# Optimization experiments

Measured on AMD Instinct MI355X. Metric: run time of the kernel, lower is better.

The kernel has to match this reference:

```python
import jax, jax.numpy as jnp
import numpy as np

B, S, D_IN, D_OUT = 8, 2048, 512, 512


def setup_inputs() -> dict:
    key = jax.random.key(0)
    ks = jax.random.split(key, 6)
    return {
        "inputs_for_keys": jax.random.normal(ks[0], (B, S, D_IN), dtype=jnp.float32),
        "inputs_for_values": jax.random.normal(ks[1], (B, S, D_IN), dtype=jnp.float32),
        "inputs_for_queries": jax.random.normal(ks[2], (B, S, D_IN), dtype=jnp.float32),
        "Wq": jax.random.normal(ks[3], (D_IN, D_OUT), dtype=jnp.float32) * 0.05,
        "Wk": jax.random.normal(ks[4], (D_IN, D_OUT), dtype=jnp.float32) * 0.05,
        "Wv": jax.random.normal(ks[5], (D_IN, D_OUT), dtype=jnp.float32) * 0.05,
    }


def reference(inputs_for_keys, inputs_for_values, inputs_for_queries, Wq, Wk, Wv):
    # Projections: [B,S,D_in] @ [D_in,D_out] -> [B,S,D_out]
    Q = inputs_for_queries @ Wq
    K = inputs_for_keys @ Wk
    V = inputs_for_values @ Wv
    d_k = K.shape[-1]
    scale = 1.0 / jnp.sqrt(jnp.float32(d_k))
    # Scores: [B,Sq,Sk]
    scores = jnp.einsum("bqd,bkd->bqk", Q, K) * scale
    # Causal mask: original adds -inf for key positions j > query i (use_mask=True)
    q_idx = jnp.arange(Q.shape[1])[:, None]
    k_idx = jnp.arange(K.shape[1])[None, :]
    scores = jnp.where(k_idx > q_idx, jnp.float32(-jnp.inf), scores)
    attn = jax.nn.softmax(scores, axis=-1)
    return jnp.einsum("bqk,bkd->bqd", attn, V)
```

## Files before the change

### kernel.cpp

```cpp
#include <hip/hip_runtime.h>
#include <hip/hip_bf16.h>

typedef __bf16 bf16;
typedef __bf16 bf16x4 __attribute__((ext_vector_type(4)));
typedef __bf16 bf16x8 __attribute__((ext_vector_type(8)));
typedef float f32x4 __attribute__((ext_vector_type(4)));
typedef float f32x16 __attribute__((ext_vector_type(16)));

#define NB 8
#define NS 2048
#define ND 512

static __device__ __forceinline__ f32x4 mfma16(bf16x8 a, bf16x8 b, f32x4 c) {
  return __builtin_amdgcn_mfma_f32_16x16x32_bf16(a, b, c, 0, 0, 0);
}
static __device__ __forceinline__ f32x16 mfma32(bf16x8 a, bf16x8 b, f32x16 c) {
  return __builtin_amdgcn_mfma_f32_32x32x16_bf16(a, b, c, 0, 0, 0);
}
static __device__ __forceinline__ void async16(const bf16* g, bf16* l) {
  __builtin_amdgcn_global_load_lds((const __attribute__((address_space(1))) void*)g,
                                   (__attribute__((address_space(3))) void*)l, 16, 0, 0);
}

#define WAVE_VM0() asm volatile("s_waitcnt vmcnt(0)" ::: "memory")
#define BLK_BAR() do { asm volatile("s_waitcnt lgkmcnt(0)" ::: "memory"); \
  __builtin_amdgcn_s_barrier(); __builtin_amdgcn_sched_barrier(0); } while (0)

__global__ void wconv_kernel(const float* __restrict__ Wq,
                             const float* __restrict__ Wk,
                             const float* __restrict__ Wv,
                             bf16* __restrict__ Wt) {
  __shared__ float buf[64][65];
  const int z = blockIdx.z;
  const float* W = (z == 0) ? Wq : (z == 1) ? Wk : Wv;
  const float scale = (z == 0) ? 0.063763537f : 1.0f;
  const int k0 = blockIdx.x * 64, n0 = blockIdx.y * 64;
  const int t = threadIdx.x;
#pragma unroll
  for (int i = 0; i < 16; ++i) {
    int idx = i * 256 + t;
    int kk = idx >> 6, nn = idx & 63;
    buf[kk][nn] = W[(size_t)(k0 + kk) * 512 + n0 + nn];
  }
  __syncthreads();
#pragma unroll
  for (int i = 0; i < 16; ++i) {
    int idx = i * 256 + t;
    int nn = idx >> 6, kk = idx & 63;
    Wt[(size_t)z * 262144 + (size_t)(n0 + nn) * 512 + k0 + (kk ^ ((nn & 7) << 3))] =
        (bf16)(buf[kk][nn] * scale);
  }
}

__launch_bounds__(256)
__global__ void proj_kernel(const float* __restrict__ Xq,
                            const float* __restrict__ Xk,
                            const float* __restrict__ Xv,
                            const bf16* __restrict__ Wt,
                            bf16* __restrict__ Cq,
                            bf16* __restrict__ Ck,
                            bf16* __restrict__ Cv) {
  __shared__ bf16 As[2][128][72];
  __shared__ bf16 WsL[2][8192];
  const int z = blockIdx.z;
  const float* A = (z == 0) ? Xq : (z == 1) ? Xk : Xv;
  const bf16* Wz = Wt + (size_t)z * 262144;
  bf16* C = (z == 0) ? Cq : (z == 1) ? Ck : Cv;

  const int t = threadIdx.x;
  const int lane = t & 63;
  const int w = t >> 6;
  const int wr = w >> 1, wc = w & 1;
  const int bxr = blockIdx.x;
  const int mt = (bxr & 7) * 16 + (bxr >> 3);
  const int bm = mt * 128;
  const int bn = blockIdx.y * 128;
  const int r0 = t >> 4, seg = t & 15;

  f32x4 acc[4][4] = {};
  float4 ar[8];

  auto loadA = [&](int kc) {
#pragma unroll
    for (int p = 0; p < 8; ++p)
      ar[p] = *(const float4*)(A + (size_t)(bm + p * 16 + r0) * 512 + kc * 64 + seg * 4);
  };
  auto writeA = [&](int bufi) {
#pragma unroll
    for (int p = 0; p < 8; ++p) {
      bf16x4 o = {(bf16)ar[p].x, (bf16)ar[p].y, (bf16)ar[p].z, (bf16)ar[p].w};
      *(bf16x4*)&As[bufi][p * 16 + r0][seg * 4] = o;
    }
  };
  auto issueW = [&](int kc, int bufi) {
    const int n = t >> 3, sg8 = t & 7;
#pragma unroll
    for (int i = 0; i < 4; ++i)
      async16(Wz + (size_t)(bn + i * 32 + n) * 512 + kc * 64 + sg8 * 8,
              &WsL[bufi][(i * 32 + n) * 64 + sg8 * 8]);
  };

  loadA(0);
  WAVE_VM0();
  writeA(0);
  issueW(0, 0);
  loadA(1);
  asm volatile("s_waitcnt vmcnt(8) lgkmcnt(0)" ::: "memory");
  __builtin_amdgcn_s_barrier();
  __builtin_amdgcn_sched_barrier(0);

#pragma unroll
  for (int kc = 0; kc < 8; ++kc) {
    const int c = kc & 1;
    if (kc < 7) issueW(kc + 1, c ^ 1);
    const int arow = lane & 15, kq = (lane >> 4) * 8;
#pragma unroll
    for (int kk = 0; kk < 2; ++kk) {
      bf16x8 af[4], bfr[4];
#pragma unroll
      for (int mi = 0; mi < 4; ++mi)
        af[mi] = *(const bf16x8*)&As[c][wr * 64 + mi * 16 + arow][kk * 32 + kq];
#pragma unroll
      for (int ni = 0; ni < 4; ++ni) {
        int n = wc * 64 + ni * 16 + arow;
        bfr[ni] = *(const bf16x8*)&WsL[c][n * 64 + ((kk * 32 + kq) ^ ((n & 7) << 3))];
      }
#pragma unroll
      for (int mi = 0; mi < 4; ++mi)
#pragma unroll
        for (int ni = 0; ni < 4; ++ni)
          acc[mi][ni] = mfma16(af[mi], bfr[ni], acc[mi][ni]);
    }
    if (kc < 7) {
      asm volatile("s_waitcnt vmcnt(4)" ::: "memory");
      writeA(c ^ 1);
      if (kc < 6) {
        loadA(kc + 2);
        asm volatile("s_waitcnt vmcnt(8) lgkmcnt(0)" ::: "memory");
      } else {
        asm volatile("s_waitcnt vmcnt(0) lgkmcnt(0)" ::: "memory");
      }
      __builtin_amdgcn_s_barrier();
      __builtin_amdgcn_sched_barrier(0);
    }
  }

  const int row0 = (lane >> 4) * 4, col = lane & 15;
#pragma unroll
  for (int mi = 0; mi < 4; ++mi)
#pragma unroll
    for (int ni = 0; ni < 4; ++ni) {
      int cg = bn + wc * 64 + ni * 16 + col;
#pragma unroll
      for (int j = 0; j < 4; ++j) {
        int rg = bm + wr * 64 + mi * 16 + row0 + j;
        bf16 o = (bf16)acc[mi][ni][j];
        if (z == 0) {
          C[(size_t)rg * ND + cg] = o;
        } else if (z == 1) {
          C[(size_t)rg * ND + (cg ^ ((rg & 7) << 3))] = o;
        } else {
          int bb = rg >> 11, s = rg & 2047;
          int ss = (s & ~63) | ((s & 63) ^ ((cg & 7) << 3));
          C[(size_t)bb * (ND * NS) + (size_t)cg * NS + ss] = o;
        }
      }
    }
}

__launch_bounds__(512, 2)
__global__ void attn_kernel(const bf16* __restrict__ Qg,
                            const bf16* __restrict__ Kg,
                            const bf16* __restrict__ Vtg,
                            bf16* __restrict__ Pn,
                            float* __restrict__ Mp,
                            float* __restrict__ Lp) {
  __shared__ bf16 Ks[64][512];
  __shared__ bf16 Vts[512][64];
  __shared__ bf16 Sx[64][68];
  __shared__ bf16 Ps[2][64][76];
  __shared__ float r_lds[2][64];
  __shared__ float l_lds[64];

  const int t = threadIdx.x;
  const int lane = t & 63;
  const int w = t >> 6;
  const int l31 = lane & 31, lhi = lane >> 5;
  const int wq = w & 3;
  const bool isQK = w < 4;
  const int qh = wq & 1, skh = wq >> 1;
  const int dofs = wq * 128;

  const int id = blockIdx.x;
  const int b = id & 7;
  const int qt = 31 - ((id >> 3) & 31);
  const int h = id >> 8;
  const int q0 = qt * 64;
  const int nt = qt + 1, mid = (nt + 1) >> 1;
  const int t_begin = h ? mid : 0;
  const int t_end = h ? nt : mid;
  const int NT = t_end - t_begin;
  const int pidx = (h * 8 + b) * 32 + qt;

  const bf16* Qb = Qg + (size_t)b * NS * ND;
  const bf16* Kb = Kg + (size_t)b * NS * ND;
  const bf16* Vb = Vtg + (size_t)b * ND * NS;

  if (isQK) {
    const int ql = qh * 32 + l31;
    const int qg = q0 + ql;
    bf16x8 qf[16];
    float m_run = -1e30f, l_run = 0.0f;
    if (NT > 0) {
      const bf16* qrow = Qb + (size_t)qg * ND + skh * 256 + lhi * 8;
#pragma unroll
      for (int kc = 0; kc < 16; ++kc) qf[kc] = *(const bf16x8*)(qrow + kc * 16);
#pragma unroll
      for (int i = 0; i < 16; ++i)
        async16(Kb + (size_t)(t_begin * 64 + wq * 16 + i) * ND + lane * 8,
                &Ks[wq * 16 + i][0]);
    }
    for (int s = 0; s <= NT; ++s) {
      const int it = t_begin + s;
      f32x16 s0 = {}, s1 = {};
      if (s < NT) WAVE_VM0();
      BLK_BAR();
      if (s < NT) {
        __builtin_amdgcn_s_setprio(1);
#pragma unroll
        for (int kc = 0; kc < 16; ++kc) {
          const int colk = (skh * 256 + kc * 16 + lhi * 8) ^ ((l31 & 7) << 3);
          bf16x8 kf0 = *(const bf16x8*)&Ks[l31][colk];
          bf16x8 kf1 = *(const bf16x8*)&Ks[32 + l31][colk];
          s0 = mfma32(kf0, qf[kc], s0);
          s1 = mfma32(kf1, qf[kc], s1);
        }
        __builtin_amdgcn_s_setprio(0);
        if (skh) {
#pragma unroll
          for (int jg = 0; jg < 4; ++jg) {
            bf16x4 a = {(bf16)s0[jg * 4 + 0], (bf16)s0[jg * 4 + 1],
                        (bf16)s0[jg * 4 + 2], (bf16)s0[jg * 4 + 3]};
            bf16x4 c = {(bf16)s1[jg * 4 + 0], (bf16)s1[jg * 4 + 1],
                        (bf16)s1[jg * 4 + 2], (bf16)s1[jg * 4 + 3]};
            *(bf16x4*)&Sx[ql][jg * 8 + 4 * lhi] = a;
            *(bf16x4*)&Sx[ql][32 + jg * 8 + 4 * lhi] = c;
          }
        }
      }
      BLK_BAR();
      if (s < NT) {
        if (it + 1 < t_end) {
#pragma unroll
          for (int i = 0; i < 16; ++i)
            async16(Kb + (size_t)((it + 1) * 64 + wq * 16 + i) * ND + lane * 8,
                    &Ks[wq * 16 + i][0]);
        }
        if (!skh) {
          float v[32];
#pragma unroll
          for (int jg = 0; jg < 4; ++jg) {
            bf16x4 a = *(const bf16x4*)&Sx[ql][jg * 8 + 4 * lhi];
            bf16x4 c = *(const bf16x4*)&Sx[ql][32 + jg * 8 + 4 * lhi];
#pragma unroll
            for (int e = 0; e < 4; ++e) {
              v[jg * 4 + e] = s0[jg * 4 + e] + (float)a[e];
              v[16 + jg * 4 + e] = s1[jg * 4 + e] + (float)c[e];
            }
          }
          if (it == qt) {
            const int k0 = it * 64;
#pragma unroll
            for (int j = 0; j < 16; ++j) {
              int kv = k0 + (j & 3) + 8 * (j >> 2) + 4 * lhi;
              if (kv > qg) v[j] = -1e30f;
              if (kv + 32 > qg) v[16 + j] = -1e30f;
            }
          }
          float mx = v[0];
#pragma unroll
          for (int j = 1; j < 32; ++j) mx = fmaxf(mx, v[j]);
          mx = fmaxf(mx, __shfl_xor(mx, 32));
          float mn = fmaxf(m_run, mx);
          float rr = exp2f(m_run - mn);
          float sum = 0.0f;
#pragma unroll
          for (int j = 0; j < 32; ++j) { v[j] = exp2f(v[j] - mn); sum += v[j]; }
          sum += __shfl_xor(sum, 32);
          m_run = mn;
          l_run = l_run * rr + sum;
          if (lhi == 0) r_lds[it & 1][ql] = rr;
#pragma unroll
          for (int jg = 0; jg < 4; ++jg) {
            bf16x4 a = {(bf16)v[jg * 4 + 0], (bf16)v[jg * 4 + 1],
                        (bf16)v[jg * 4 + 2], (bf16)v[jg * 4 + 3]};
            bf16x4 c = {(bf16)v[16 + jg * 4 + 0], (bf16)v[16 + jg * 4 + 1],
                        (bf16)v[16 + jg * 4 + 2], (bf16)v[16 + jg * 4 + 3]};
            *(bf16x4*)&Ps[it & 1][ql][jg * 8 + 4 * lhi] = a;
            *(bf16x4*)&Ps[it & 1][ql][32 + jg * 8 + 4 * lhi] = c;
          }
        }
      }
    }
    if (!skh && lhi == 0) {
      Mp[pidx * 64 + ql] = m_run;
      Lp[pidx * 64 + ql] = l_run;
      l_lds[ql] = l_run;
    }
    BLK_BAR();
  } else {
    f32x16 acc[2][4] = {};
    if (NT > 0) {
#pragma unroll
      for (int i = 0; i < 16; ++i) {
        int d = dofs + i * 8 + (lane >> 3);
        async16(Vb + (size_t)d * NS + t_begin * 64 + (lane & 7) * 8,
                &Vts[dofs + i * 8][0]);
      }
    }
    for (int s = 0; s <= NT; ++s) {
      const int it = t_begin + s;
      if (s >= 1) WAVE_VM0();
      BLK_BAR();
      bf16x8 paf[2][4];
      if (s >= 1) {
        const int bb = (it - 1) & 1;
#pragma unroll
        for (int qb = 0; qb < 2; ++qb)
#pragma unroll
          for (int j = 0; j < 16; ++j) {
            float rr = r_lds[bb][qb * 32 + (j & 3) + 8 * (j >> 2) + 4 * lhi];
#pragma unroll
            for (int dt = 0; dt < 4; ++dt) acc[qb][dt][j] *= rr;
          }
#pragma unroll
        for (int qb = 0; qb < 2; ++qb)
#pragma unroll
          for (int kc = 0; kc < 4; ++kc)
            paf[qb][kc] = *(const bf16x8*)&Ps[bb][qb * 32 + l31][kc * 16 + lhi * 8];
        __builtin_amdgcn_s_setprio(1);
#pragma unroll
        for (int dt = 0; dt < 2; ++dt) {
          const int d = dofs + dt * 32 + l31;
          const int swzv = (d & 7) << 3;
#pragma unroll
          for (int kc = 0; kc < 4; ++kc) {
            bf16x8 vf = *(const bf16x8*)&Vts[d][(kc * 16 + lhi * 8) ^ swzv];
            acc[0][dt] = mfma32(paf[0][kc], vf, acc[0][dt]);
            acc[1][dt] = mfma32(paf[1][kc], vf, acc[1][dt]);
          }
        }
        __builtin_amdgcn_s_setprio(0);
      }
      BLK_BAR();
      if (s >= 1) {
        __builtin_amdgcn_s_setprio(1);
#pragma unroll
        for (int dt = 2; dt < 4; ++dt) {
          const int d = dofs + dt * 32 + l31;
          const int swzv = (d & 7) << 3;
#pragma unroll
          for (int kc = 0; kc < 4; ++kc) {
            bf16x8 vf = *(const bf16x8*)&Vts[d][(kc * 16 + lhi * 8) ^ swzv];
            acc[0][dt] = mfma32(paf[0][kc], vf, acc[0][dt]);
            acc[1][dt] = mfma32(paf[1][kc], vf, acc[1][dt]);
          }
        }
        __builtin_amdgcn_s_setprio(0);
        asm volatile("s_waitcnt lgkmcnt(0)" ::: "memory");
        if (it < t_end) {
#pragma unroll
          for (int i = 0; i < 16; ++i) {
            int d = dofs + i * 8 + (lane >> 3);
            async16(Vb + (size_t)d * NS + it * 64 + (lane & 7) * 8,
                    &Vts[dofs + i * 8][0]);
          }
        }
      }
    }
    BLK_BAR();
    bf16* Ob = Pn + (size_t)pidx * 64 * ND;
#pragma unroll
    for (int qb = 0; qb < 2; ++qb)
#pragma unroll
      for (int j = 0; j < 16; ++j) {
        const int row = qb * 32 + (j & 3) + 8 * (j >> 2) + 4 * lhi;
        float lv = l_lds[row];
        float linv = (lv > 0.0f) ? 1.0f / lv : 0.0f;
#pragma unroll
        for (int dt = 0; dt < 4; ++dt)
          Ob[(size_t)row * ND + dofs + dt * 32 + l31] = (bf16)(acc[qb][dt][j] * linv);
      }
  }
}

__global__ void combine_kernel(const bf16* __restrict__ Pn,
                               const float* __restrict__ Mp,
                               const float* __restrict__ Lp,
                               float* __restrict__ Out) {
  const int total = NB * NS * ND / 4;
  for (int v = blockIdx.x * 256 + threadIdx.x; v < total; v += gridDim.x * 256) {
    int e = v * 4;
    int d = e & 511;
    int s = (e >> 9) & 2047;
    int bb = e >> 20;
    int qt = s >> 6, r = s & 63;
    int p0 = (bb * 32 + qt) * 64 + r;
    int p1 = ((8 + bb) * 32 + qt) * 64 + r;
    float m0 = Mp[p0], l0 = Lp[p0], m1 = Mp[p1], l1 = Lp[p1];
    float M = fmaxf(m0, m1);
    float w0 = l0 * exp2f(m0 - M), w1 = l1 * exp2f(m1 - M);
    float inv = 1.0f / (w0 + w1);
    bf16x4 o0 = *(const bf16x4*)(Pn + (size_t)p0 * ND + d);
    bf16x4 o1 = *(const bf16x4*)(Pn + (size_t)p1 * ND + d);
    f32x4 o;
    o[0] = (w0 * (float)o0[0] + w1 * (float)o1[0]) * inv;
    o[1] = (w0 * (float)o0[1] + w1 * (float)o1[1]) * inv;
    o[2] = (w0 * (float)o0[2] + w1 * (float)o1[2]) * inv;
    o[3] = (w0 * (float)o0[3] + w1 * (float)o1[3]) * inv;
    __builtin_nontemporal_store(o, (f32x4*)(Out + e));
  }
}

extern "C" void kernel_launch(void* const* d_in, const int* in_sizes, int n_in,
                              void* d_out, int out_size, void* d_ws, size_t ws_size,
                              hipStream_t stream) {
  const float* Xk = (const float*)d_in[0];
  const float* Xv = (const float*)d_in[1];
  const float* Xq = (const float*)d_in[2];
  const float* Wq = (const float*)d_in[3];
  const float* Wk = (const float*)d_in[4];
  const float* Wv = (const float*)d_in[5];
  float* Out = (float*)d_out;

  char* ws = (char*)d_ws;
  bf16* Qb = (bf16*)(ws);
  bf16* Kb = (bf16*)(ws + (size_t)16 * 1024 * 1024);
  bf16* Vt = (bf16*)(ws + (size_t)32 * 1024 * 1024);
  bf16* Wt = (bf16*)(ws + (size_t)48 * 1024 * 1024);
  bf16* Pn = (bf16*)(ws + (size_t)50 * 1024 * 1024);
  float* Mp = (float*)(ws + (size_t)82 * 1024 * 1024);
  float* Lp = (float*)(ws + (size_t)82 * 1024 * 1024 + 131072);

  wconv_kernel<<<dim3(8, 8, 3), 256, 0, stream>>>(Wq, Wk, Wv, Wt);
  proj_kernel<<<dim3(128, 4, 3), 256, 0, stream>>>(Xq, Xk, Xv, Wt, Qb, Kb, Vt);
  attn_kernel<<<512, 512, 0, stream>>>(Qb, Kb, Vt, Pn, Mp, Lp);
  combine_kernel<<<2048, 256, 0, stream>>>(Pn, Mp, Lp, Out);
}
```

Before: 146.8 us.

## Split only long query tiles across blocks and repartition QK waves by key half

The work split now depends on tile length. Query tiles 0-15 run as a single block that writes fp32 output directly. Tiles 16-31 are split into two KV halves that still go through the combine kernel, so the grid drops to 384 blocks and combine only handles the upper half of the sequence. The QK waves now each compute a 32-key half over the full head dimension and exchange per-row max and sum through LDS. This removes the bf16 partial-score exchange and the serial softmax on half the waves. Each QK wave now keeps twice as many Q fragments in registers, and the launch bound drops to one block per SM, which may reduce occupancy.

```diff
diff --git a/kernel.cpp b/kernel.cpp
--- a/kernel.cpp
+++ b/kernel.cpp
@@ -168,17 +168,18 @@
     }
 }
 
-__launch_bounds__(512, 2)
+__launch_bounds__(512, 1)
 __global__ void attn_kernel(const bf16* __restrict__ Qg,
                             const bf16* __restrict__ Kg,
                             const bf16* __restrict__ Vtg,
+                            float* __restrict__ Out,
                             bf16* __restrict__ Pn,
                             float* __restrict__ Mp,
                             float* __restrict__ Lp) {
   __shared__ bf16 Ks[64][512];
   __shared__ bf16 Vts[512][64];
-  __shared__ bf16 Sx[64][68];
   __shared__ bf16 Ps[2][64][76];
+  __shared__ float2 Mx[2][64];
   __shared__ float r_lds[2][64];
   __shared__ float l_lds[64];
 
@@ -188,19 +189,24 @@
   const int l31 = lane & 31, lhi = lane >> 5;
   const int wq = w & 3;
   const bool isQK = w < 4;
-  const int qh = wq & 1, skh = wq >> 1;
+  const int qh = wq & 1, kvh = wq >> 1;
   const int dofs = wq * 128;
 
   const int id = blockIdx.x;
   const int b = id & 7;
-  const int qt = 31 - ((id >> 3) & 31);
-  const int h = id >> 8;
+  const int g = id >> 3;
+  const int j3 = g / 3, r3 = g - 3 * j3;
+  int qt, t_begin, t_end, mode;
+  if (r3 == 0) { qt = 15 - j3; t_begin = 0; t_end = qt + 1; mode = 0; }
+  else {
+    qt = 31 - j3;
+    int mid = (qt + 2) >> 1;
+    if (r3 == 1) { t_begin = 0; t_end = mid; mode = 1; }
+    else { t_begin = mid; t_end = qt + 1; mode = 2; }
+  }
   const int q0 = qt * 64;
-  const int nt = qt + 1, mid = (nt + 1) >> 1;
-  const int t_begin = h ? mid : 0;
-  const int t_end = h ? nt : mid;
   const int NT = t_end - t_begin;
-  const int pidx = (h * 8 + b) * 32 + qt;
+  const int pidx = ((mode == 2 ? 8 : 0) + b) * 32 + qt;
 
   const bf16* Qb = Qg + (size_t)b * NS * ND;
   const bf16* Kb = Kg + (size_t)b * NS * ND;
@@ -209,44 +215,49 @@
   if (isQK) {
     const int ql = qh * 32 + l31;
     const int qg = q0 + ql;
-    bf16x8 qf[16];
+    bf16x8 qf[32];
     float m_run = -1e30f, l_run = 0.0f;
-    if (NT > 0) {
-      const bf16* qrow = Qb + (size_t)qg * ND + skh * 256 + lhi * 8;
-#pragma unroll
-      for (int kc = 0; kc < 16; ++kc) qf[kc] = *(const bf16x8*)(qrow + kc * 16);
+    {
+      const bf16* qrow = Qb + (size_t)qg * ND + lhi * 8;
+#pragma unroll
+      for (int kc = 0; kc < 32; ++kc) qf[kc] = *(const bf16x8*)(qrow + kc * 16);
 #pragma unroll
       for (int i = 0; i < 16; ++i)
         async16(Kb + (size_t)(t_begin * 64 + wq * 16 + i) * ND + lane * 8,
                 &Ks[wq * 16 + i][0]);
     }
+    const int swz = (l31 & 7) << 3;
+    const int krow = kvh * 32 + l31;
     for (int s = 0; s <= NT; ++s) {
       const int it = t_begin + s;
-      f32x16 s0 = {}, s1 = {};
+      f32x16 sacc = {};
       if (s < NT) WAVE_VM0();
       BLK_BAR();
+      float m_loc = -1e30f, sum_loc = 0.0f, p[16];
       if (s < NT) {
         __builtin_amdgcn_s_setprio(1);
 #pragma unroll
-        for (int kc = 0; kc < 16; ++kc) {
-          const int colk = (skh * 256 + kc * 16 + lhi * 8) ^ ((l31 & 7) << 3);
-          bf16x8 kf0 = *(const bf16x8*)&Ks[l31][colk];
-          bf16x8 kf1 = *(const bf16x8*)&Ks[32 + l31][colk];
-          s0 = mfma32(kf0, qf[kc], s0);
-          s1 = mfma32(kf1, qf[kc], s1);
+        for (int kc = 0; kc < 32; ++kc) {
+          bf16x8 kf = *(const bf16x8*)&Ks[krow][(kc * 16 + lhi * 8) ^ swz];
+          sacc = mfma32(kf, qf[kc], sacc);
         }
         __builtin_amdgcn_s_setprio(0);
-        if (skh) {
-#pragma unroll
-          for (int jg = 0; jg < 4; ++jg) {
-            bf16x4 a = {(bf16)s0[jg * 4 + 0], (bf16)s0[jg * 4 + 1],
-                        (bf16)s0[jg * 4 + 2], (bf16)s0[jg * 4 + 3]};
-            bf16x4 c = {(bf16)s1[jg * 4 + 0], (bf16)s1[jg * 4 + 1],
-                        (bf16)s1[jg * 4 + 2], (bf16)s1[jg * 4 + 3]};
-            *(bf16x4*)&Sx[ql][jg * 8 + 4 * lhi] = a;
-            *(bf16x4*)&Sx[ql][32 + jg * 8 + 4 * lhi] = c;
-          }
-        }
+        float v[16];
+#pragma unroll
+        for (int j = 0; j < 16; ++j) v[j] = sacc[j];
+        if (it == qt && mode != 1) {
+          const int kvb = it * 64 + kvh * 32;
+#pragma unroll
+          for (int j = 0; j < 16; ++j)
+            if (kvb + (j & 3) + 8 * (j >> 2) + 4 * lhi > qg) v[j] = -1e30f;
+        }
+#pragma unroll
+        for (int j = 0; j < 16; ++j) m_loc = fmaxf(m_loc, v[j]);
+        m_loc = fmaxf(m_loc, __shfl_xor(m_loc, 32));
+#pragma unroll
+        for (int j = 0; j < 16; ++j) { p[j] = exp2f(v[j] - m_loc); sum_loc += p[j]; }
+        sum_loc += __shfl_xor(sum_loc, 32);
+        if (lhi == 0) Mx[kvh][ql] = {m_loc, sum_loc};
       }
       BLK_BAR();
       if (s < NT) {
@@ -256,61 +267,30 @@
             async16(Kb + (size_t)((it + 1) * 64 + wq * 16 + i) * ND + lane * 8,
                     &Ks[wq * 16 + i][0]);
         }
-        if (!skh) {
-          float v[32];
-#pragma unroll
-          for (int jg = 0; jg < 4; ++jg) {
-            bf16x4 a = *(const bf16x4*)&Sx[ql][jg * 8 + 4 * lhi];
-            bf16x4 c = *(const bf16x4*)&Sx[ql][32 + jg * 8 + 4 * lhi];
-#pragma unroll
-            for (int e = 0; e < 4; ++e) {
-              v[jg * 4 + e] = s0[jg * 4 + e] + (float)a[e];
-              v[16 + jg * 4 + e] = s1[jg * 4 + e] + (float)c[e];
-            }
-          }
-          if (it == qt) {
-            const int k0 = it * 64;
-#pragma unroll
-            for (int j = 0; j < 16; ++j) {
-              int kv = k0 + (j & 3) + 8 * (j >> 2) + 4 * lhi;
-              if (kv > qg) v[j] = -1e30f;
-              if (kv + 32 > qg) v[16 + j] = -1e30f;
-            }
-          }
-          float mx = v[0];
-#pragma unroll
-          for (int j = 1; j < 32; ++j) mx = fmaxf(mx, v[j]);
-          mx = fmaxf(mx, __shfl_xor(mx, 32));
-          float mn = fmaxf(m_run, mx);
-          float rr = exp2f(m_run - mn);
-          float sum = 0.0f;
-#pragma unroll
-          for (int j = 0; j < 32; ++j) { v[j] = exp2f(v[j] - mn); sum += v[j]; }
-          sum += __shfl_xor(sum, 32);
-          m_run = mn;
-          l_run = l_run * rr + sum;
-          if (lhi == 0) r_lds[it & 1][ql] = rr;
-#pragma unroll
-          for (int jg = 0; jg < 4; ++jg) {
-            bf16x4 a = {(bf16)v[jg * 4 + 0], (bf16)v[jg * 4 + 1],
-                        (bf16)v[jg * 4 + 2], (bf16)v[jg * 4 + 3]};
-            bf16x4 c = {(bf16)v[16 + jg * 4 + 0], (bf16)v[16 + jg * 4 + 1],
-                        (bf16)v[16 + jg * 4 + 2], (bf16)v[16 + jg * 4 + 3]};
-            *(bf16x4*)&Ps[it & 1][ql][jg * 8 + 4 * lhi] = a;
-            *(bf16x4*)&Ps[it & 1][ql][32 + jg * 8 + 4 * lhi] = c;
-          }
-        }
-      }
-    }
-    if (!skh && lhi == 0) {
-      Mp[pidx * 64 + ql] = m_run;
-      Lp[pidx * 64 + ql] = l_run;
+        float2 oth = Mx[kvh ^ 1][ql];
+        float m_tile = fmaxf(m_loc, oth.x);
+        float mn = fmaxf(m_run, m_tile);
+        float e_own = exp2f(m_loc - mn);
+        float rr = exp2f(m_run - mn);
+        l_run = l_run * rr + sum_loc * e_own + oth.y * exp2f(oth.x - mn);
+        if (kvh == 0 && lhi == 0) r_lds[it & 1][ql] = rr;
+        m_run = mn;
+#pragma unroll
+        for (int jg = 0; jg < 4; ++jg) {
+          bf16x4 pv = {(bf16)(p[jg * 4 + 0] * e_own), (bf16)(p[jg * 4 + 1] * e_own),
+                       (bf16)(p[jg * 4 + 2] * e_own), (bf16)(p[jg * 4 + 3] * e_own)};
+          *(bf16x4*)&Ps[it & 1][ql][kvh * 32 + jg * 8 + 4 * lhi] = pv;
+        }
+      }
+    }
+    if (kvh == 0 && lhi == 0) {
       l_lds[ql] = l_run;
+      if (mode != 0) { Mp[pidx * 64 + ql] = m_run; Lp[pidx * 64 + ql] = l_run; }
     }
     BLK_BAR();
   } else {
     f32x16 acc[2][4] = {};
-    if (NT > 0) {
+    {
 #pragma unroll
       for (int i = 0; i < 16; ++i) {
         int d = dofs + i * 8 + (lane >> 3);
@@ -379,18 +359,34 @@
       }
     }
     BLK_BAR();
-    bf16* Ob = Pn + (size_t)pidx * 64 * ND;
-#pragma unroll
-    for (int qb = 0; qb < 2; ++qb)
-#pragma unroll
-      for (int j = 0; j < 16; ++j) {
-        const int row = qb * 32 + (j & 3) + 8 * (j >> 2) + 4 * lhi;
-        float lv = l_lds[row];
-        float linv = (lv > 0.0f) ? 1.0f / lv : 0.0f;
-#pragma unroll
-        for (int dt = 0; dt < 4; ++dt)
-          Ob[(size_t)row * ND + dofs + dt * 32 + l31] = (bf16)(acc[qb][dt][j] * linv);
-      }
+    if (mode == 0) {
+      float* Ob = Out + (size_t)b * NS * ND;
+#pragma unroll
+      for (int qb = 0; qb < 2; ++qb)
+#pragma unroll
+        for (int j = 0; j < 16; ++j) {
+          const int row = qb * 32 + (j & 3) + 8 * (j >> 2) + 4 * lhi;
+          float lv = l_lds[row];
+          float linv = (lv > 0.0f) ? 1.0f / lv : 0.0f;
+#pragma unroll
+          for (int dt = 0; dt < 4; ++dt)
+            __builtin_nontemporal_store(acc[qb][dt][j] * linv,
+                &Ob[(size_t)(q0 + row) * ND + dofs + dt * 32 + l31]);
+        }
+    } else {
+      bf16* Ob = Pn + (size_t)pidx * 64 * ND;
+#pragma unroll
+      for (int qb = 0; qb < 2; ++qb)
+#pragma unroll
+        for (int j = 0; j < 16; ++j) {
+          const int row = qb * 32 + (j & 3) + 8 * (j >> 2) + 4 * lhi;
+          float lv = l_lds[row];
+          float linv = (lv > 0.0f) ? 1.0f / lv : 0.0f;
+#pragma unroll
+          for (int dt = 0; dt < 4; ++dt)
+            Ob[(size_t)row * ND + dofs + dt * 32 + l31] = (bf16)(acc[qb][dt][j] * linv);
+        }
+    }
   }
 }
 
@@ -398,12 +394,13 @@
                                const float* __restrict__ Mp,
                                const float* __restrict__ Lp,
                                float* __restrict__ Out) {
-  const int total = NB * NS * ND / 4;
+  const int total = NB * NS * ND / 8;
   for (int v = blockIdx.x * 256 + threadIdx.x; v < total; v += gridDim.x * 256) {
     int e = v * 4;
     int d = e & 511;
-    int s = (e >> 9) & 2047;
-    int bb = e >> 20;
+    int shi = (e >> 9) & 1023;
+    int bb = e >> 19;
+    int s = 1024 + shi;
     int qt = s >> 6, r = s & 63;
     int p0 = (bb * 32 + qt) * 64 + r;
     int p1 = ((8 + bb) * 32 + qt) * 64 + r;
@@ -418,7 +415,7 @@
     o[1] = (w0 * (float)o0[1] + w1 * (float)o1[1]) * inv;
     o[2] = (w0 * (float)o0[2] + w1 * (float)o1[2]) * inv;
     o[3] = (w0 * (float)o0[3] + w1 * (float)o1[3]) * inv;
-    __builtin_nontemporal_store(o, (f32x4*)(Out + e));
+    __builtin_nontemporal_store(o, (f32x4*)(Out + (size_t)bb * NS * ND + (size_t)s * ND + d));
   }
 }
 
@@ -444,6 +441,6 @@
 
   wconv_kernel<<<dim3(8, 8, 3), 256, 0, stream>>>(Wq, Wk, Wv, Wt);
   proj_kernel<<<dim3(128, 4, 3), 256, 0, stream>>>(Xq, Xk, Xv, Wt, Qb, Kb, Vt);
-  attn_kernel<<<512, 512, 0, stream>>>(Qb, Kb, Vt, Pn, Mp, Lp);
-  combine_kernel<<<2048, 256, 0, stream>>>(Pn, Mp, Lp, Out);
-}
+  attn_kernel<<<384, 512, 0, stream>>>(Qb, Kb, Vt, Out, Pn, Mp, Lp);
+  combine_kernel<<<1024, 256, 0, stream>>>(Pn, Mp, Lp, Out);
+}
```

Result: no change. 149.7 us (+1.9%).

## Split only long causal query tiles and write short tiles directly to output

Applied to the files above, without the earlier changes.

Work is now partitioned so that the 16 short query tiles per batch run in a single block and write fp32 output directly. Only the 16 long tiles are split in two across KV ranges and merged by the combine kernel, which now handles just the upper half of the sequence. The grid shrinks from 512 to 384 blocks, and launch bounds drop to one block per CU to allow more registers. This removes split-and-combine traffic for half the tiles and balances per-block work, at the risk of lower occupancy and different scheduling behaviour.

```diff
diff --git a/kernel.cpp b/kernel.cpp
--- a/kernel.cpp
+++ b/kernel.cpp
@@ -168,10 +168,11 @@
     }
 }
 
-__launch_bounds__(512, 2)
+__launch_bounds__(512, 1)
 __global__ void attn_kernel(const bf16* __restrict__ Qg,
                             const bf16* __restrict__ Kg,
                             const bf16* __restrict__ Vtg,
+                            float* __restrict__ Out,
                             bf16* __restrict__ Pn,
                             float* __restrict__ Mp,
                             float* __restrict__ Lp) {
@@ -193,14 +194,19 @@
 
   const int id = blockIdx.x;
   const int b = id & 7;
-  const int qt = 31 - ((id >> 3) & 31);
-  const int h = id >> 8;
+  const int g = id >> 3;
+  const int j3 = g / 3, r3 = g - 3 * j3;
+  int qt, t_begin, t_end, mode;
+  if (r3 == 0) { qt = 15 - j3; t_begin = 0; t_end = qt + 1; mode = 0; }
+  else {
+    qt = 31 - j3;
+    int mid = (qt + 2) >> 1;
+    if (r3 == 1) { t_begin = 0; t_end = mid; mode = 1; }
+    else { t_begin = mid; t_end = qt + 1; mode = 2; }
+  }
   const int q0 = qt * 64;
-  const int nt = qt + 1, mid = (nt + 1) >> 1;
-  const int t_begin = h ? mid : 0;
-  const int t_end = h ? nt : mid;
   const int NT = t_end - t_begin;
-  const int pidx = (h * 8 + b) * 32 + qt;
+  const int pidx = ((mode == 2 ? 8 : 0) + b) * 32 + qt;
 
   const bf16* Qb = Qg + (size_t)b * NS * ND;
   const bf16* Kb = Kg + (size_t)b * NS * ND;
@@ -211,7 +217,7 @@
     const int qg = q0 + ql;
     bf16x8 qf[16];
     float m_run = -1e30f, l_run = 0.0f;
-    if (NT > 0) {
+    {
       const bf16* qrow = Qb + (size_t)qg * ND + skh * 256 + lhi * 8;
 #pragma unroll
       for (int kc = 0; kc < 16; ++kc) qf[kc] = *(const bf16x8*)(qrow + kc * 16);
@@ -303,14 +309,13 @@
       }
     }
     if (!skh && lhi == 0) {
-      Mp[pidx * 64 + ql] = m_run;
-      Lp[pidx * 64 + ql] = l_run;
       l_lds[ql] = l_run;
+      if (mode != 0) { Mp[pidx * 64 + ql] = m_run; Lp[pidx * 64 + ql] = l_run; }
     }
     BLK_BAR();
   } else {
     f32x16 acc[2][4] = {};
-    if (NT > 0) {
+    {
 #pragma unroll
       for (int i = 0; i < 16; ++i) {
         int d = dofs + i * 8 + (lane >> 3);
@@ -379,18 +384,34 @@
       }
     }
     BLK_BAR();
-    bf16* Ob = Pn + (size_t)pidx * 64 * ND;
-#pragma unroll
-    for (int qb = 0; qb < 2; ++qb)
-#pragma unroll
-      for (int j = 0; j < 16; ++j) {
-        const int row = qb * 32 + (j & 3) + 8 * (j >> 2) + 4 * lhi;
-        float lv = l_lds[row];
-        float linv = (lv > 0.0f) ? 1.0f / lv : 0.0f;
-#pragma unroll
-        for (int dt = 0; dt < 4; ++dt)
-          Ob[(size_t)row * ND + dofs + dt * 32 + l31] = (bf16)(acc[qb][dt][j] * linv);
-      }
+    if (mode == 0) {
+      float* Ob = Out + (size_t)b * NS * ND;
+#pragma unroll
+      for (int qb = 0; qb < 2; ++qb)
+#pragma unroll
+        for (int j = 0; j < 16; ++j) {
+          const int row = qb * 32 + (j & 3) + 8 * (j >> 2) + 4 * lhi;
+          float lv = l_lds[row];
+          float linv = (lv > 0.0f) ? 1.0f / lv : 0.0f;
+#pragma unroll
+          for (int dt = 0; dt < 4; ++dt)
+            __builtin_nontemporal_store(acc[qb][dt][j] * linv,
+                &Ob[(size_t)(q0 + row) * ND + dofs + dt * 32 + l31]);
+        }
+    } else {
+      bf16* Ob = Pn + (size_t)pidx * 64 * ND;
+#pragma unroll
+      for (int qb = 0; qb < 2; ++qb)
+#pragma unroll
+        for (int j = 0; j < 16; ++j) {
+          const int row = qb * 32 + (j & 3) + 8 * (j >> 2) + 4 * lhi;
+          float lv = l_lds[row];
+          float linv = (lv > 0.0f) ? 1.0f / lv : 0.0f;
+#pragma unroll
+          for (int dt = 0; dt < 4; ++dt)
+            Ob[(size_t)row * ND + dofs + dt * 32 + l31] = (bf16)(acc[qb][dt][j] * linv);
+        }
+    }
   }
 }
 
@@ -398,12 +419,13 @@
                                const float* __restrict__ Mp,
                                const float* __restrict__ Lp,
                                float* __restrict__ Out) {
-  const int total = NB * NS * ND / 4;
+  const int total = NB * NS * ND / 8;
   for (int v = blockIdx.x * 256 + threadIdx.x; v < total; v += gridDim.x * 256) {
     int e = v * 4;
     int d = e & 511;
-    int s = (e >> 9) & 2047;
-    int bb = e >> 20;
+    int shi = (e >> 9) & 1023;
+    int bb = e >> 19;
+    int s = 1024 + shi;
     int qt = s >> 6, r = s & 63;
     int p0 = (bb * 32 + qt) * 64 + r;
     int p1 = ((8 + bb) * 32 + qt) * 64 + r;
@@ -418,7 +440,7 @@
     o[1] = (w0 * (float)o0[1] + w1 * (float)o1[1]) * inv;
     o[2] = (w0 * (float)o0[2] + w1 * (float)o1[2]) * inv;
     o[3] = (w0 * (float)o0[3] + w1 * (float)o1[3]) * inv;
-    __builtin_nontemporal_store(o, (f32x4*)(Out + e));
+    __builtin_nontemporal_store(o, (f32x4*)(Out + (size_t)bb * NS * ND + (size_t)s * ND + d));
   }
 }
 
@@ -444,6 +466,6 @@
 
   wconv_kernel<<<dim3(8, 8, 3), 256, 0, stream>>>(Wq, Wk, Wv, Wt);
   proj_kernel<<<dim3(128, 4, 3), 256, 0, stream>>>(Xq, Xk, Xv, Wt, Qb, Kb, Vt);
-  attn_kernel<<<512, 512, 0, stream>>>(Qb, Kb, Vt, Pn, Mp, Lp);
-  combine_kernel<<<2048, 256, 0, stream>>>(Pn, Mp, Lp, Out);
-}
+  attn_kernel<<<384, 512, 0, stream>>>(Qb, Kb, Vt, Out, Pn, Mp, Lp);
+  combine_kernel<<<1024, 256, 0, stream>>>(Pn, Mp, Lp, Out);
+}
```

Result: slower. 152.4 us (+3.8%).
